# Kernel tuning notes

Measured on AMD Instinct MI355X. Metric: run time of the kernel, lower is better.

The kernel has to match this reference:

```python
import jax, jax.numpy as jnp
import numpy as np

B, T, D, H, L = 256, 512, 32, 128, 32


def gru_cell(x, h, Wih, Whh, bih, bhh):
    # PyTorch GRU cell: gates ordered (r, z, n)
    gi = x @ Wih.T + bih
    gh = h @ Whh.T + bhh
    ir, iz, inn = jnp.split(gi, 3, axis=-1)
    hr, hz, hn = jnp.split(gh, 3, axis=-1)
    r = jax.nn.sigmoid(ir + hr)
    z = jax.nn.sigmoid(iz + hz)
    n = jnp.tanh(inn + r * hn)
    return (1.0 - z) * n + z * h


def run_dir(x, lengths, Wih, Whh, bih, bhh):
    # Unidirectional GRU over padded batch; masked updates emulate packed sequences:
    # carry at the end equals the hidden state at each sequence's last valid step.
    Bb, Tt, _ = x.shape
    xT = jnp.swapaxes(x, 0, 1)                                   # [T,B,Din]
    mask = (jnp.arange(Tt)[:, None] < lengths[None, :])[:, :, None]  # [T,B,1]
    h0 = jnp.zeros((Bb, Whh.shape[1]), x.dtype)

    def step(h, inp):
        x_t, m = inp
        h_new = gru_cell(x_t, h, Wih, Whh, bih, bhh)
        h = jnp.where(m, h_new, h)
        return h, jnp.where(m, h_new, jnp.zeros_like(h_new))

    h_last, out = jax.lax.scan(step, h0, (xT, mask))
    return jnp.swapaxes(out, 0, 1), h_last


def reverse_seq(x, lengths):
    # Reverse each sequence within its own valid length (positions >= length are junk,
    # callers mask them out).
    Tt = x.shape[1]
    idx = jnp.clip(lengths[:, None] - 1 - jnp.arange(Tt)[None, :], 0)
    return jnp.take_along_axis(x, idx[:, :, None], axis=1)


def vrae_forward(x, eps, enc_Wih0, enc_Whh0, enc_bih0, enc_bhh0,
                 enc_Wih12, enc_Whh12, enc_bih12, enc_bhh12,
                 dec_Wih0, dec_Whh0, dec_bih0, dec_bhh0,
                 dec_Wih1, dec_Whh1, dec_bih1, dec_bhh1,
                 W_mean, b_mean, W_logvar, b_logvar,
                 W_z2h, b_z2h, W_out, b_out, lengths):
    Bb, Tt, _ = x.shape
    valid = (jnp.arange(Tt)[None, :] < lengths[:, None])[:, :, None].astype(x.dtype)

    # --- 3-layer bidirectional encoder (packed-sequence semantics) ---
    seq = x
    for l in range(3):
        if l == 0:
            pf = (enc_Wih0[0], enc_Whh0[0], enc_bih0[0], enc_bhh0[0])
            pb = (enc_Wih0[1], enc_Whh0[1], enc_bih0[1], enc_bhh0[1])
        else:
            pf = (enc_Wih12[l-1, 0], enc_Whh12[l-1, 0], enc_bih12[l-1, 0], enc_bhh12[l-1, 0])
            pb = (enc_Wih12[l-1, 1], enc_Whh12[l-1, 1], enc_bih12[l-1, 1], enc_bhh12[l-1, 1])
        out_f, h_f = run_dir(seq, lengths, *pf)
        out_b_rev, h_b = run_dir(reverse_seq(seq, lengths), lengths, *pb)
        out_b = reverse_seq(out_b_rev, lengths) * valid
        seq = jnp.concatenate([out_f, out_b], axis=-1)

    # hidden[-2] = last-layer forward final, hidden[-1] = last-layer backward final
    hcat = jnp.concatenate([h_f, h_b], axis=-1)                  # [B, 2H]
    mean = hcat @ W_mean.T + b_mean
    logvar = hcat @ W_logvar.T + b_logvar
    z = mean + jnp.exp(0.5 * logvar) * eps

    h_init = jnp.tanh(z @ W_z2h.T + b_z2h)                       # repeated over layers

    def dec_step(carry, _):
        d_in, h1, h2 = carry
        h1n = gru_cell(d_in, h1, dec_Wih0, dec_Whh0, dec_bih0, dec_bhh0)
        h2n = gru_cell(h1n, h2, dec_Wih1, dec_Whh1, dec_bih1, dec_bhh1)
        pred = h2n @ W_out.T + b_out
        return (pred, h1n, h2n), pred

    init = (jnp.zeros((Bb, x.shape[2]), x.dtype), h_init, h_init)
    _, preds = jax.lax.scan(dec_step, init, None, length=Tt)     # [T,B,D]
    reconstruction = jnp.swapaxes(preds, 0, 1)                   # [B,T,D]
    return reconstruction, mean, logvar


def setup_inputs() -> dict:
    key = jax.random.key(0)
    ks = jax.random.split(key, 32)
    s = 0.1
    inp = {}
    inp["x"] = jax.random.normal(ks[0], (B, T, D), jnp.float32)
    lengths = jnp.sort(jax.random.randint(ks[1], (B,), 1, T + 1))[::-1]
    inp["lengths"] = lengths.at[0].set(T).astype(jnp.int32)      # sorted desc, max == T
    inp["eps"] = jax.random.normal(ks[2], (B, L), jnp.float32)
    # encoder layer 0 (input D), stacked over directions [fwd, bwd]
    inp["enc_Wih0"] = jax.random.normal(ks[3], (2, 3 * H, D)) * s
    inp["enc_Whh0"] = jax.random.normal(ks[4], (2, 3 * H, H)) * s
    inp["enc_bih0"] = jax.random.normal(ks[5], (2, 3 * H)) * s
    inp["enc_bhh0"] = jax.random.normal(ks[6], (2, 3 * H)) * s
    # encoder layers 1..2 (input 2H), [layer, dir, ...]
    inp["enc_Wih12"] = jax.random.normal(ks[7], (2, 2, 3 * H, 2 * H)) * s
    inp["enc_Whh12"] = jax.random.normal(ks[8], (2, 2, 3 * H, H)) * s
    inp["enc_bih12"] = jax.random.normal(ks[9], (2, 2, 3 * H)) * s
    inp["enc_bhh12"] = jax.random.normal(ks[10], (2, 2, 3 * H)) * s
    # decoder layer 0 (input D) and layer 1 (input H)
    inp["dec_Wih0"] = jax.random.normal(ks[11], (3 * H, D)) * s
    inp["dec_Whh0"] = jax.random.normal(ks[12], (3 * H, H)) * s
    inp["dec_bih0"] = jax.random.normal(ks[13], (3 * H,)) * s
    inp["dec_bhh0"] = jax.random.normal(ks[14], (3 * H,)) * s
    inp["dec_Wih1"] = jax.random.normal(ks[15], (3 * H, H)) * s
    inp["dec_Whh1"] = jax.random.normal(ks[16], (3 * H, H)) * s
    inp["dec_bih1"] = jax.random.normal(ks[17], (3 * H,)) * s
    inp["dec_bhh1"] = jax.random.normal(ks[18], (3 * H,)) * s
    # linears
    inp["W_mean"] = jax.random.normal(ks[19], (L, 2 * H)) * s
    inp["b_mean"] = jax.random.normal(ks[20], (L,)) * s
    inp["W_logvar"] = jax.random.normal(ks[21], (L, 2 * H)) * s
    inp["b_logvar"] = jax.random.normal(ks[22], (L,)) * s
    inp["W_z2h"] = jax.random.normal(ks[23], (H, L)) * s
    inp["b_z2h"] = jax.random.normal(ks[24], (H,)) * s
    inp["W_out"] = jax.random.normal(ks[25], (D, H)) * s
    inp["b_out"] = jax.random.normal(ks[26], (D,)) * s
    return inp


def reference(x, lengths, eps, enc_Wih0, enc_Whh0, enc_bih0, enc_bhh0,
              enc_Wih12, enc_Whh12, enc_bih12, enc_bhh12,
              dec_Wih0, dec_Whh0, dec_bih0, dec_bhh0,
              dec_Wih1, dec_Whh1, dec_bih1, dec_bhh1,
              W_mean, b_mean, W_logvar, b_logvar,
              W_z2h, b_z2h, W_out, b_out):
    return vrae_forward(x, eps, enc_Wih0, enc_Whh0, enc_bih0, enc_bhh0,
                        enc_Wih12, enc_Whh12, enc_bih12, enc_bhh12,
                        dec_Wih0, dec_Whh0, dec_bih0, dec_bhh0,
                        dec_Wih1, dec_Whh1, dec_bih1, dec_bhh1,
                        W_mean, b_mean, W_logvar, b_logvar,
                        W_z2h, b_z2h, W_out, b_out, lengths)
```

## Files before the change

kernel.cpp:

```cpp
#include <hip/hip_runtime.h>
#include <hip/hip_bf16.h>


typedef __bf16 bf16;
typedef __bf16 bf16x8 __attribute__((ext_vector_type(8)));
typedef float f32x4 __attribute__((ext_vector_type(4)));

#define MFMA(a,b,c) __builtin_amdgcn_mfma_f32_16x16x32_bf16((a),(b),(c),0,0,0)
#define Z4 (f32x4){0.f,0.f,0.f,0.f}

__device__ __forceinline__ float sigm_(float x){ return 1.f/(1.f+__expf(-x)); }
__device__ __forceinline__ float tanh_(float x){
  x = fminf(15.f, fmaxf(-15.f, x));
  float e = __expf(2.f*x);
  return (e-1.f)/(e+1.f);
}
__device__ __forceinline__ float fin_(float v){ return (v - v == 0.0f) ? v : 0.0f; }
__device__ __forceinline__ void pina_(bf16x8 &v){ asm volatile("" : "+a"(v)); }

struct PrepJobs {
  const float* src[9];
  bf16* hi[9];
  bf16* lo[9];
  int n[9];
};

__global__ void prep_w(PrepJobs J){
  const int stride = gridDim.x*blockDim.x;
  const int t0 = blockIdx.x*blockDim.x + threadIdx.x;
  for (int j=0;j<9;++j){
    const float* __restrict__ s = J.src[j];
    bf16* __restrict__ h = J.hi[j];
    bf16* __restrict__ l = J.lo[j];
    const int n = J.n[j];
    for (int i=t0;i<n;i+=stride){
      float v = fin_(s[i]);
      bf16 hh = (bf16)v;
      h[i] = hh;
      l[i] = (bf16)(v - (float)hh);
    }
  }
}

template<int KIN, bool F32IN>
__global__ __launch_bounds__(512)
__attribute__((amdgpu_waves_per_eu(2, 2)))
void enc_rec(const void* __restrict__ seqIn_,
             bf16* __restrict__ seqOut,
             const bf16* __restrict__ WihHi_, const bf16* __restrict__ WihLo_,
             const bf16* __restrict__ WhhHi_, const bf16* __restrict__ WhhLo_,
             const float* __restrict__ bih_, const float* __restrict__ bhh_,
             const int* __restrict__ lengths,
             float* __restrict__ hFo, float* __restrict__ hBo)
{
  constexpr int NKS  = KIN/32;
  constexpr int XSTR = F32IN ? 40 : 264;
  constexpr int XPL  = 16*XSTR;
  constexpr int XSLOT= (F32IN?2:1)*XPL;
  const int tid = threadIdx.x;
  const int wave = tid>>6;
  const int lh   = tid&15;
  const int quad = (tid>>4)&3;
  const int dir  = blockIdx.x>>4;
  const int b0   = (blockIdx.x&15)*16;

  const bf16* __restrict__ WihHi = WihHi_ + (size_t)dir*384*KIN;
  const bf16* __restrict__ WihLo = WihLo_ + (size_t)dir*384*KIN;
  const bf16* __restrict__ WhhHi = WhhHi_ + (size_t)dir*384*128;
  const bf16* __restrict__ WhhLo = WhhLo_ + (size_t)dir*384*128;
  const float* __restrict__ bih = bih_ + dir*384;
  const float* __restrict__ bhh = bhh_ + dir*384;

  __shared__ bf16 hHi[16*136], hLo[16*136];
  __shared__ bf16 xb[4*XSLOT];

  const int jc = wave*16 + lh;
  const int cR = jc, cZ = 128+jc, cN = 256+jc;

  bf16x8 wRH[4],wRL[4],wZH[4],wZL[4],wNH[4],wNL[4];
#pragma unroll
  for (int ks=0;ks<4;++ks){
    const int o = ks*32 + quad*8;
    wRH[ks]=*(const bf16x8*)(WhhHi+(size_t)cR*128+o); wRL[ks]=*(const bf16x8*)(WhhLo+(size_t)cR*128+o);
    wZH[ks]=*(const bf16x8*)(WhhHi+(size_t)cZ*128+o); wZL[ks]=*(const bf16x8*)(WhhLo+(size_t)cZ*128+o);
    wNH[ks]=*(const bf16x8*)(WhhHi+(size_t)cN*128+o); wNL[ks]=*(const bf16x8*)(WhhLo+(size_t)cN*128+o);
    pina_(wRH[ks]); pina_(wRL[ks]); pina_(wZH[ks]); pina_(wZL[ks]); pina_(wNH[ks]); pina_(wNL[ks]);
  }
  const float bR  = bih[cR]+bhh[cR];
  const float bZc = bih[cZ]+bhh[cZ];
  const float bNi = bih[cN];
  const float bNh = bhh[cN];

  int lenRow[4];
#pragma unroll
  for (int r=0;r<4;++r) lenRow[r] = lengths[b0 + quad*4 + r];
  const int lenA = lengths[b0+lh];
  const int Tmax = lengths[b0];
  const int TT   = (Tmax+3)&~3;

  const int wrow = (tid>>4)&15;
  const int wcol = (tid&15)*8;
  const int lenW = lengths[b0 + wrow];
  const int srow = tid>>5;
  const int scol = tid&31;
  const int lenS = lengths[b0 + srow];

  for (int i=tid;i<16*136;i+=512){ hHi[i]=(bf16)0.f; hLo[i]=(bf16)0.f; }

  float hown[4] = {0.f,0.f,0.f,0.f};

  auto stage = [&](int slot, int sabs){
    int tb = dir ? (lenS-1-sabs) : sabs;
    tb = tb<0 ? 0 : (tb>511 ? 511 : tb);
    if constexpr (F32IN){
      float v = ((const float*)seqIn_)[((size_t)(b0+srow)*512+tb)*32 + scol];
      bf16 hh=(bf16)v;
      xb[slot*XSLOT + srow*XSTR + scol] = hh;
      xb[slot*XSLOT + XPL + srow*XSTR + scol] = (bf16)(v-(float)hh);
    } else {
      bf16x8 v = *(const bf16x8*)((const bf16*)seqIn_ + ((size_t)(b0+srow)*512+tb)*256 + scol*8);
      *(bf16x8*)&xb[slot*XSLOT + srow*XSTR + scol*8] = v;
    }
  };
#pragma unroll
  for (int s=0;s<4;++s) stage(s, 1+s);

  f32x4 accR[4], accZ[4], giN[4];
#pragma unroll
  for (int s=0;s<4;++s){ accR[s]=Z4; accZ[s]=Z4; giN[s]=Z4; }

  {
    int tb0 = dir ? (lenA-1) : 0; tb0 = tb0<0?0:tb0;
#pragma unroll
    for (int ks=0;ks<NKS;++ks){
      const int o = ks*32 + quad*8;
      bf16x8 axH, axL;
      if constexpr (F32IN){
        const float* ap = (const float*)seqIn_ + ((size_t)(b0+lh)*512+tb0)*KIN + o;
#pragma unroll
        for (int e=0;e<8;++e){ float v=ap[e]; bf16 hh=(bf16)v; axH[e]=hh; axL[e]=(bf16)(v-(float)hh); }
      } else {
        axH = *(const bf16x8*)((const bf16*)seqIn_ + ((size_t)(b0+lh)*512+tb0)*KIN + o);
      }
      bf16x8 bH, bL;
      bH=*(const bf16x8*)(WihHi+(size_t)cR*KIN+o); bL=*(const bf16x8*)(WihLo+(size_t)cR*KIN+o);
      accR[3]=MFMA(axH,bH,accR[3]); if constexpr(F32IN) accR[3]=MFMA(axL,bH,accR[3]); accR[3]=MFMA(axH,bL,accR[3]);
      bH=*(const bf16x8*)(WihHi+(size_t)cZ*KIN+o); bL=*(const bf16x8*)(WihLo+(size_t)cZ*KIN+o);
      accZ[3]=MFMA(axH,bH,accZ[3]); if constexpr(F32IN) accZ[3]=MFMA(axL,bH,accZ[3]); accZ[3]=MFMA(axH,bL,accZ[3]);
      bH=*(const bf16x8*)(WihHi+(size_t)cN*KIN+o); bL=*(const bf16x8*)(WihLo+(size_t)cN*KIN+o);
      giN[3]=MFMA(axH,bH,giN[3]);  if constexpr(F32IN) giN[3]=MFMA(axL,bH,giN[3]);  giN[3]=MFMA(axH,bL,giN[3]);
    }
  }
  __syncthreads();

  for (int t4=0; t4<TT; t4+=4){
#pragma unroll
    for (int p=0;p<4;++p){
      const int t = t4 + p;
      const int s = (p+3)&3;
      if (seqOut && tid<256 && t>0 && (t-1)<lenW){
        const int tp = t-1;
        const int tb = dir ? (lenW-1-tp) : tp;
        bf16x8 v = *(const bf16x8*)&hHi[wrow*136 + wcol];
        *(bf16x8*)(seqOut + ((size_t)(b0+wrow)*512 + tb)*256 + dir*128 + wcol) = v;
      }
      f32x4 gN = Z4;
#pragma unroll
      for (int ks=0;ks<4;++ks){
        bf16x8 aH = *(const bf16x8*)&hHi[lh*136 + ks*32 + quad*8];
        bf16x8 aL = *(const bf16x8*)&hLo[lh*136 + ks*32 + quad*8];
        accR[s]=MFMA(aH,wRH[ks],accR[s]); accR[s]=MFMA(aL,wRH[ks],accR[s]); accR[s]=MFMA(aH,wRL[ks],accR[s]);
        accZ[s]=MFMA(aH,wZH[ks],accZ[s]); accZ[s]=MFMA(aL,wZH[ks],accZ[s]); accZ[s]=MFMA(aH,wZL[ks],accZ[s]);
        gN     =MFMA(aH,wNH[ks],gN);      gN     =MFMA(aL,wNH[ks],gN);      gN     =MFMA(aH,wNL[ks],gN);
      }
      float hsel[4];
#pragma unroll
      for (int r=0;r<4;++r){
        float rr = sigm_(accR[s][r] + bR);
        float zz = sigm_(accZ[s][r] + bZc);
        float nn = tanh_(giN[s][r] + bNi + rr*(gN[r] + bNh));
        float hold = hown[r];
        float hnew = fin_((1.f-zz)*nn + zz*hold);
        hsel[r] = (t < lenRow[r]) ? hnew : hold;
        hown[r] = hsel[r];
      }
      if (p==0){
#pragma unroll
        for (int s2=0;s2<4;++s2){ accR[s2]=Z4; accZ[s2]=Z4; giN[s2]=Z4; }
#pragma unroll
        for (int ks=0;ks<NKS;++ks){
          const int o = ks*32 + quad*8;
          bf16x8 axH[4], axL[F32IN?4:1];
#pragma unroll
          for (int s2=0;s2<4;++s2){
            axH[s2] = *(const bf16x8*)&xb[s2*XSLOT + lh*XSTR + o];
            if constexpr (F32IN) axL[s2] = *(const bf16x8*)&xb[s2*XSLOT + XPL + lh*XSTR + o];
          }
          bf16x8 bH, bL;
          bH=*(const bf16x8*)(WihHi+(size_t)cR*KIN+o); bL=*(const bf16x8*)(WihLo+(size_t)cR*KIN+o);
#pragma unroll
          for (int s2=0;s2<4;++s2){
            accR[s2]=MFMA(axH[s2],bH,accR[s2]);
            if constexpr(F32IN) accR[s2]=MFMA(axL[s2],bH,accR[s2]);
            accR[s2]=MFMA(axH[s2],bL,accR[s2]);
          }
          bH=*(const bf16x8*)(WihHi+(size_t)cZ*KIN+o); bL=*(const bf16x8*)(WihLo+(size_t)cZ*KIN+o);
#pragma unroll
          for (int s2=0;s2<4;++s2){
            accZ[s2]=MFMA(axH[s2],bH,accZ[s2]);
            if constexpr(F32IN) accZ[s2]=MFMA(axL[s2],bH,accZ[s2]);
            accZ[s2]=MFMA(axH[s2],bL,accZ[s2]);
          }
          bH=*(const bf16x8*)(WihHi+(size_t)cN*KIN+o); bL=*(const bf16x8*)(WihLo+(size_t)cN*KIN+o);
#pragma unroll
          for (int s2=0;s2<4;++s2){
            giN[s2]=MFMA(axH[s2],bH,giN[s2]);
            if constexpr(F32IN) giN[s2]=MFMA(axL[s2],bH,giN[s2]);
            giN[s2]=MFMA(axH[s2],bL,giN[s2]);
          }
        }
      }
      __syncthreads();
#pragma unroll
      for (int r=0;r<4;++r){
        const int m = quad*4 + r;
        bf16 hi = (bf16)hsel[r];
        hHi[m*136+jc] = hi;
        hLo[m*136+jc] = (bf16)(hsel[r]-(float)hi);
      }
      if      (p==1){ stage(0, t4+5); stage(1, t4+6); }
      else if (p==2){ stage(2, t4+7); }
      else if (p==3){ stage(3, t4+8); }
      __syncthreads();
    }
  }
  if (seqOut && tid<256 && (TT-1)<lenW){
    const int tb = dir ? (lenW-1-(TT-1)) : (TT-1);
    bf16x8 v = *(const bf16x8*)&hHi[wrow*136 + wcol];
    *(bf16x8*)(seqOut + ((size_t)(b0+wrow)*512 + tb)*256 + dir*128 + wcol) = v;
  }
  float* hout = dir ? hBo : hFo;
  if (hout && tid<256){
#pragma unroll
    for (int e=0;e<8;++e){
      const int j = wcol+e;
      hout[(size_t)(b0+wrow)*128 + j] = fin_((float)hHi[wrow*136+j] + (float)hLo[wrow*136+j]);
    }
  }
}

__global__ void latent_k(const float* __restrict__ hF, const float* __restrict__ hB,
                         const float* __restrict__ eps,
                         const float* __restrict__ Wm, const float* __restrict__ bm,
                         const float* __restrict__ Wl, const float* __restrict__ bl,
                         const float* __restrict__ Wz, const float* __restrict__ bz,
                         float* __restrict__ out_mean, float* __restrict__ out_logvar,
                         float* __restrict__ hInit)
{
  const int b = blockIdx.x, tid = threadIdx.x;
  __shared__ float hc[256];
  __shared__ float mv[64];
  __shared__ float zz[32];
  for (int k=tid;k<256;k+=64) hc[k] = fin_((k<128)? hF[(size_t)b*128+k] : hB[(size_t)b*128+k-128]);
  __syncthreads();
  {
    const int i = tid & 31;
    const float* W = (tid<32)? Wm : Wl;
    float acc = (tid<32)? bm[i] : bl[i];
    for (int k=0;k<256;++k) acc += hc[k]*W[i*256+k];
    acc = fin_(acc);
    mv[tid] = acc;
    if (tid<32) out_mean[b*32+i] = acc;
    else        out_logvar[b*32+(tid-32)] = acc;
  }
  __syncthreads();
  if (tid<32) zz[tid] = fin_(mv[tid] + __expf(0.5f*mv[32+tid]) * eps[b*32+tid]);
  __syncthreads();
  for (int j=tid;j<128;j+=64){
    float a = bz[j];
    for (int k=0;k<32;++k) a += zz[k]*Wz[j*32+k];
    hInit[(size_t)b*128 + j] = tanh_(fin_(a));
  }
}

__global__ __launch_bounds__(512)
__attribute__((amdgpu_waves_per_eu(2, 2)))
void dec_rec(const float* __restrict__ hInit,
             const bf16* __restrict__ W0iH, const bf16* __restrict__ W0iL,
             const bf16* __restrict__ W0hH, const bf16* __restrict__ W0hL,
             const bf16* __restrict__ W1iH, const bf16* __restrict__ W1iL,
             const bf16* __restrict__ W1hH, const bf16* __restrict__ W1hL,
             const bf16* __restrict__ WoH,  const bf16* __restrict__ WoL,
             const float* __restrict__ bih0, const float* __restrict__ bhh0,
             const float* __restrict__ bih1, const float* __restrict__ bhh1,
             const float* __restrict__ bout,
             float* __restrict__ rec)
{
  const int tid = threadIdx.x;
  const int wave = tid>>6;
  const int lh   = tid&15;
  const int quad = (tid>>4)&3;
  const int b0 = blockIdx.x*16;
  const int jc = wave*16 + lh;
  const int cR = jc, cZ = 128+jc, cN = 256+jc;

  __shared__ bf16 h1H[16*136], h1L[16*136], h2H[16*136], h2L[16*136];
  __shared__ bf16 pH[16*40], pL[16*40];
  __shared__ bf16 w1iLds[384*128];
  __shared__ bf16 woHl[32*128], woLl[32*128];
  __shared__ bf16 w0iLds[384*32];

  const int sw1 = (jc&7)<<3;
  const int sw0 = (jc&3)<<3;
  const int swo = (lh&7)<<3;

  bf16x8 a0RH[4],a0RL[4],a0ZH[4],a0ZL[4],a0NH[4],a0NL[4];
  bf16x8 a1RH[4],a1RL[4],a1ZH[4],a1ZL[4],a1NH[4],a1NL[4];
#pragma unroll
  for (int ks=0;ks<4;++ks){
    const int o = ks*32 + quad*8;
    a0RH[ks]=*(const bf16x8*)(W0hH+(size_t)cR*128+o); a0RL[ks]=*(const bf16x8*)(W0hL+(size_t)cR*128+o);
    a0ZH[ks]=*(const bf16x8*)(W0hH+(size_t)cZ*128+o); a0ZL[ks]=*(const bf16x8*)(W0hL+(size_t)cZ*128+o);
    a0NH[ks]=*(const bf16x8*)(W0hH+(size_t)cN*128+o); a0NL[ks]=*(const bf16x8*)(W0hL+(size_t)cN*128+o);
    a1RH[ks]=*(const bf16x8*)(W1hH+(size_t)cR*128+o); a1RL[ks]=*(const bf16x8*)(W1hL+(size_t)cR*128+o);
    a1ZH[ks]=*(const bf16x8*)(W1hH+(size_t)cZ*128+o); a1ZL[ks]=*(const bf16x8*)(W1hL+(size_t)cZ*128+o);
    a1NH[ks]=*(const bf16x8*)(W1hH+(size_t)cN*128+o); a1NL[ks]=*(const bf16x8*)(W1hL+(size_t)cN*128+o);
    pina_(a0RH[ks]); pina_(a0RL[ks]); pina_(a0ZH[ks]); pina_(a0ZL[ks]); pina_(a0NH[ks]); pina_(a0NL[ks]);
    pina_(a1RH[ks]); pina_(a1RL[ks]); pina_(a1ZH[ks]); pina_(a1ZL[ks]); pina_(a1NH[ks]); pina_(a1NL[ks]);
  }
  const float b1R = bih0[cR]+bhh0[cR], b1Z = bih0[cZ]+bhh0[cZ], b1Ni = bih0[cN], b1Nh = bhh0[cN];
  const float b2R = bih1[cR]+bhh1[cR], b2Z = bih1[cZ]+bhh1[cZ], b2Ni = bih1[cN], b2Nh = bhh1[cN];
  const float bo = (wave<2) ? bout[wave*16+lh] : 0.f;

  for (int i=tid; i<384*16; i+=512){
    const int rr = i>>4, k8 = (i&15)*8;
    *(bf16x8*)&w1iLds[rr*128 + (k8 ^ ((rr&7)<<3))] = *(const bf16x8*)(W1iH + (size_t)rr*128 + k8);
  }
  for (int i=tid; i<32*16; i+=512){
    const int rr = i>>4, k8 = (i&15)*8;
    const int c = rr*128 + (k8 ^ ((rr&7)<<3));
    *(bf16x8*)&woHl[c] = *(const bf16x8*)(WoH + (size_t)rr*128 + k8);
    *(bf16x8*)&woLl[c] = *(const bf16x8*)(WoL + (size_t)rr*128 + k8);
  }
  for (int i=tid; i<384*4; i+=512){
    const int rr = i>>2, k8 = (i&3)*8;
    *(bf16x8*)&w0iLds[rr*32 + (k8 ^ ((rr&3)<<3))] = *(const bf16x8*)(W0iH + (size_t)rr*32 + k8);
  }
  float h1own[4], h2own[4];
#pragma unroll
  for (int r=0;r<4;++r){
    float v = fin_(hInit[(size_t)(b0+quad*4+r)*128 + jc]);
    h1own[r]=v; h2own[r]=v;
  }
  if (tid < 256){
    const int row = (tid>>4)&15;
    const int c0  = (tid&15)*8;
#pragma unroll
    for (int e=0;e<8;++e){
      const int j = c0+e;
      float v = fin_(hInit[(size_t)(b0+row)*128 + j]);
      bf16 hi=(bf16)v, lo=(bf16)(v-(float)hi);
      h1H[row*136+j]=hi; h1L[row*136+j]=lo;
      h2H[row*136+j]=hi; h2L[row*136+j]=lo;
    }
  }
  for (int i=tid;i<16*40;i+=512){ pH[i]=(bf16)0.f; pL[i]=(bf16)0.f; }
  __syncthreads();

  f32x4 c1R, c1Z, c1Nh, c2R, c2Z, c2Nh;

  auto ghpre = [&](){
    c1R=Z4; c1Z=Z4; c1Nh=Z4; c2R=Z4; c2Z=Z4; c2Nh=Z4;
#pragma unroll
    for (int ks=0;ks<4;++ks){
      const int o = ks*32 + quad*8;
      bf16x8 aH = *(const bf16x8*)&h1H[lh*136 + o];
      bf16x8 aL = *(const bf16x8*)&h1L[lh*136 + o];
      c1R =MFMA(aH,a0RH[ks],c1R);  c1R =MFMA(aL,a0RH[ks],c1R);  c1R =MFMA(aH,a0RL[ks],c1R);
      c1Z =MFMA(aH,a0ZH[ks],c1Z);  c1Z =MFMA(aL,a0ZH[ks],c1Z);  c1Z =MFMA(aH,a0ZL[ks],c1Z);
      c1Nh=MFMA(aH,a0NH[ks],c1Nh); c1Nh=MFMA(aL,a0NH[ks],c1Nh); c1Nh=MFMA(aH,a0NL[ks],c1Nh);
    }
#pragma unroll
    for (int ks=0;ks<4;++ks){
      const int o = ks*32 + quad*8;
      bf16x8 aH = *(const bf16x8*)&h2H[lh*136 + o];
      bf16x8 aL = *(const bf16x8*)&h2L[lh*136 + o];
      c2R =MFMA(aH,a1RH[ks],c2R);  c2R =MFMA(aL,a1RH[ks],c2R);  c2R =MFMA(aH,a1RL[ks],c2R);
      c2Z =MFMA(aH,a1ZH[ks],c2Z);  c2Z =MFMA(aL,a1ZH[ks],c2Z);  c2Z =MFMA(aH,a1ZL[ks],c2Z);
      c2Nh=MFMA(aH,a1NH[ks],c2Nh); c2Nh=MFMA(aL,a1NH[ks],c2Nh); c2Nh=MFMA(aH,a1NL[ks],c2Nh);
    }
  };
  ghpre();

  for (int t=0;t<512;++t){
    {
      f32x4 c1Ni = Z4;
      bf16x8 aP0 = *(const bf16x8*)&pH[lh*40 + quad*8];
      bf16x8 aP1 = *(const bf16x8*)&pL[lh*40 + quad*8];
      const int o = quad*8;
      bf16x8 bH,bL;
      bH=*(const bf16x8*)&w0iLds[cR*32 + (o^sw0)]; bL=*(const bf16x8*)(W0iL+(size_t)cR*32+o);
      c1R=MFMA(aP0,bH,c1R); c1R=MFMA(aP1,bH,c1R); c1R=MFMA(aP0,bL,c1R);
      bH=*(const bf16x8*)&w0iLds[cZ*32 + (o^sw0)]; bL=*(const bf16x8*)(W0iL+(size_t)cZ*32+o);
      c1Z=MFMA(aP0,bH,c1Z); c1Z=MFMA(aP1,bH,c1Z); c1Z=MFMA(aP0,bL,c1Z);
      bH=*(const bf16x8*)&w0iLds[cN*32 + (o^sw0)]; bL=*(const bf16x8*)(W0iL+(size_t)cN*32+o);
      c1Ni=MFMA(aP0,bH,c1Ni); c1Ni=MFMA(aP1,bH,c1Ni); c1Ni=MFMA(aP0,bL,c1Ni);
#pragma unroll
      for (int r=0;r<4;++r){
        const int m = quad*4+r;
        float rr = sigm_(c1R[r] + b1R);
        float z  = sigm_(c1Z[r] + b1Z);
        float nn = tanh_(c1Ni[r] + b1Ni + rr*(c1Nh[r] + b1Nh));
        float hnew = fin_((1.f-z)*nn + z*h1own[r]);
        h1own[r] = hnew;
        bf16 hi=(bf16)hnew;
        h1H[m*136+jc]=hi; h1L[m*136+jc]=(bf16)(hnew-(float)hi);
      }
    }
    __syncthreads();
    {
      f32x4 c2Ni = Z4;
#pragma unroll
      for (int ks=0;ks<4;++ks){
        const int o = ks*32 + quad*8;
        bf16x8 aH = *(const bf16x8*)&h1H[lh*136 + o];
        bf16x8 aL = *(const bf16x8*)&h1L[lh*136 + o];
        bf16x8 bH,bL;
        bH=*(const bf16x8*)&w1iLds[cR*128+(o^sw1)]; bL=*(const bf16x8*)(W1iL+(size_t)cR*128+o);
        c2R=MFMA(aH,bH,c2R); c2R=MFMA(aL,bH,c2R); c2R=MFMA(aH,bL,c2R);
        bH=*(const bf16x8*)&w1iLds[cZ*128+(o^sw1)]; bL=*(const bf16x8*)(W1iL+(size_t)cZ*128+o);
        c2Z=MFMA(aH,bH,c2Z); c2Z=MFMA(aL,bH,c2Z); c2Z=MFMA(aH,bL,c2Z);
        bH=*(const bf16x8*)&w1iLds[cN*128+(o^sw1)]; bL=*(const bf16x8*)(W1iL+(size_t)cN*128+o);
        c2Ni=MFMA(aH,bH,c2Ni); c2Ni=MFMA(aL,bH,c2Ni); c2Ni=MFMA(aH,bL,c2Ni);
      }
#pragma unroll
      for (int r=0;r<4;++r){
        const int m = quad*4+r;
        float rr = sigm_(c2R[r] + b2R);
        float z  = sigm_(c2Z[r] + b2Z);
        float nn = tanh_(c2Ni[r] + b2Ni + rr*(c2Nh[r] + b2Nh));
        float hnew = fin_((1.f-z)*nn + z*h2own[r]);
        h2own[r] = hnew;
        bf16 hi=(bf16)hnew;
        h2H[m*136+jc]=hi; h2L[m*136+jc]=(bf16)(hnew-(float)hi);
      }
    }
    __syncthreads();
    if (wave<2){
      f32x4 po=Z4;
#pragma unroll
      for (int ks=0;ks<4;++ks){
        const int o = ks*32 + quad*8;
        bf16x8 oH = *(const bf16x8*)&h2H[lh*136 + o];
        bf16x8 oL = *(const bf16x8*)&h2L[lh*136 + o];
        const int wc = (wave*16+lh)*128 + (o^swo);
        bf16x8 bH = *(const bf16x8*)&woHl[wc];
        bf16x8 bL = *(const bf16x8*)&woLl[wc];
        po=MFMA(oH,bH,po); po=MFMA(oL,bH,po); po=MFMA(oH,bL,po);
      }
#pragma unroll
      for (int r=0;r<4;++r){
        const int m = quad*4+r;
        float pv = fin_(po[r]+bo);
        rec[((size_t)(b0+m)*512 + t)*32 + wave*16+lh] = pv;
        bf16 hi=(bf16)pv;
        pH[m*40 + wave*16+lh]=hi; pL[m*40 + wave*16+lh]=(bf16)(pv-(float)hi);
      }
    }
    if (t+1 < 512) ghpre();
    __syncthreads();
  }
}

extern "C" void kernel_launch(void* const* d_in, const int* in_sizes, int n_in,
                              void* d_out, int out_size, void* d_ws, size_t ws_size,
                              hipStream_t stream)
{
  const float* x       = (const float*)d_in[0];
  const int*   lengths = (const int*)d_in[1];
  const float* eps     = (const float*)d_in[2];
  const float* eWih0   = (const float*)d_in[3];
  const float* eWhh0   = (const float*)d_in[4];
  const float* ebih0   = (const float*)d_in[5];
  const float* ebhh0   = (const float*)d_in[6];
  const float* eWih12  = (const float*)d_in[7];
  const float* eWhh12  = (const float*)d_in[8];
  const float* ebih12  = (const float*)d_in[9];
  const float* ebhh12  = (const float*)d_in[10];
  const float* dWih0   = (const float*)d_in[11];
  const float* dWhh0   = (const float*)d_in[12];
  const float* dbih0   = (const float*)d_in[13];
  const float* dbhh0   = (const float*)d_in[14];
  const float* dWih1   = (const float*)d_in[15];
  const float* dWhh1   = (const float*)d_in[16];
  const float* dbih1   = (const float*)d_in[17];
  const float* dbhh1   = (const float*)d_in[18];
  const float* Wm      = (const float*)d_in[19];
  const float* bm      = (const float*)d_in[20];
  const float* Wl      = (const float*)d_in[21];
  const float* bl      = (const float*)d_in[22];
  const float* Wz      = (const float*)d_in[23];
  const float* bz      = (const float*)d_in[24];
  const float* Wo      = (const float*)d_in[25];
  const float* bo      = (const float*)d_in[26];

  char* ws = (char*)d_ws;
  bf16* P     = (bf16*)ws;
  bf16* seqA  = (bf16*)(ws + (size_t)(4<<20));
  bf16* seqB  = (bf16*)(ws + (size_t)(68<<20));
  float* hF    = (float*)seqA;
  float* hB    = hF + 256*128;
  float* hInit = hB + 256*128;

  const size_t O_eWih0  = 0;
  const size_t O_eWhh0  = 49152;
  const size_t O_eWih12 = 245760;
  const size_t O_eWhh12 = 1032192;
  const size_t O_dWih0  = 1425408;
  const size_t O_dWhh0  = 1449984;
  const size_t O_dWih1  = 1548288;
  const size_t O_dWhh1  = 1646592;
  const size_t O_Wout   = 1744896;

  float* out   = (float*)d_out;
  float* rec   = out;
  float* omean = out + (size_t)4194304;
  float* ologv = omean + 8192;

  size_t zoff = (size_t)(4<<20);
  size_t zbytes = (size_t)(128<<20);
  if (zoff + zbytes > ws_size) zbytes = (ws_size > zoff)? ws_size - zoff : 0;
  hipMemsetAsync(ws + zoff, 0, zbytes, stream);

  PrepJobs J;
  const float* srcs[9] = {eWih0, eWhh0, eWih12, eWhh12, dWih0, dWhh0, dWih1, dWhh1, Wo};
  const size_t offs[9] = {O_eWih0,O_eWhh0,O_eWih12,O_eWhh12,O_dWih0,O_dWhh0,O_dWih1,O_dWhh1,O_Wout};
  const int    ns[9]   = {24576, 98304, 393216, 196608, 12288, 49152, 49152, 49152, 4096};
  for (int j=0;j<9;++j){ J.src[j]=srcs[j]; J.hi[j]=P+offs[j]; J.lo[j]=P+offs[j]+ns[j]; J.n[j]=ns[j]; }
  prep_w<<<256, 256, 0, stream>>>(J);

  dim3 blk(512);

  enc_rec<32,true><<<32, blk, 0, stream>>>(x, seqA,
      P+O_eWih0, P+O_eWih0+24576, P+O_eWhh0, P+O_eWhh0+98304,
      ebih0, ebhh0, lengths, nullptr, nullptr);
  enc_rec<256,false><<<32, blk, 0, stream>>>(seqA, seqB,
      P+O_eWih12, P+O_eWih12+393216, P+O_eWhh12, P+O_eWhh12+196608,
      ebih12, ebhh12, lengths, nullptr, nullptr);
  enc_rec<256,false><<<32, blk, 0, stream>>>(seqB, nullptr,
      P+O_eWih12+196608, P+O_eWih12+393216+196608,
      P+O_eWhh12+98304,  P+O_eWhh12+196608+98304,
      ebih12+768, ebhh12+768, lengths, hF, hB);
  latent_k<<<256, 64, 0, stream>>>(hF, hB, eps, Wm, bm, Wl, bl, Wz, bz,
                                   omean, ologv, hInit);
  dec_rec<<<16, blk, 0, stream>>>(hInit,
      P+O_dWih0, P+O_dWih0+12288, P+O_dWhh0, P+O_dWhh0+49152,
      P+O_dWih1, P+O_dWih1+49152, P+O_dWhh1, P+O_dWhh1+49152,
      P+O_Wout,  P+O_Wout+4096,
      dbih0, dbhh0, dbih1, dbhh1, bo, rec);
}
```

Baseline: 9.967 ms.

## Double-buffer encoder hidden state in LDS and rebalance decoder weight registers

The encoder's shared hidden-state buffers become ping-pong double buffers. Each step reads one copy and writes the other, which removes one of the two block-wide barriers per timestep. In the decoder, some layer-0 recurrent weight fragments are pinned to VGPRs instead of AGPRs, and the N-gate low fragment is reloaded from global memory inside ghpre. This is meant to relieve register pressure, at the cost of an extra global load per k-step.

```diff
diff --git a/kernel.cpp b/kernel.cpp
--- a/kernel.cpp
+++ b/kernel.cpp
@@ -16,6 +16,7 @@
   return (e-1.f)/(e+1.f);
 }
 __device__ __forceinline__ float fin_(float v){ return (v - v == 0.0f) ? v : 0.0f; }
+__device__ __forceinline__ void pinv_(bf16x8 &v){ asm volatile("" : "+v"(v)); }
 __device__ __forceinline__ void pina_(bf16x8 &v){ asm volatile("" : "+a"(v)); }
 
 struct PrepJobs {
@@ -71,7 +72,7 @@
   const float* __restrict__ bih = bih_ + dir*384;
   const float* __restrict__ bhh = bhh_ + dir*384;
 
-  __shared__ bf16 hHi[16*136], hLo[16*136];
+  __shared__ bf16 hHi[2][16*136], hLo[2][16*136];
   __shared__ bf16 xb[4*XSLOT];
 
   const int jc = wave*16 + lh;
@@ -105,7 +106,7 @@
   const int scol = tid&31;
   const int lenS = lengths[b0 + srow];
 
-  for (int i=tid;i<16*136;i+=512){ hHi[i]=(bf16)0.f; hLo[i]=(bf16)0.f; }
+  for (int i=tid;i<2*16*136;i+=512){ hHi[0][i]=(bf16)0.f; hLo[0][i]=(bf16)0.f; }
 
   float hown[4] = {0.f,0.f,0.f,0.f};
 
@@ -158,17 +159,19 @@
     for (int p=0;p<4;++p){
       const int t = t4 + p;
       const int s = (p+3)&3;
+      const int rp = (p+1)&1;
+      const int wp = p&1;
       if (seqOut && tid<256 && t>0 && (t-1)<lenW){
         const int tp = t-1;
         const int tb = dir ? (lenW-1-tp) : tp;
-        bf16x8 v = *(const bf16x8*)&hHi[wrow*136 + wcol];
+        bf16x8 v = *(const bf16x8*)&hHi[rp][wrow*136 + wcol];
         *(bf16x8*)(seqOut + ((size_t)(b0+wrow)*512 + tb)*256 + dir*128 + wcol) = v;
       }
       f32x4 gN = Z4;
 #pragma unroll
       for (int ks=0;ks<4;++ks){
-        bf16x8 aH = *(const bf16x8*)&hHi[lh*136 + ks*32 + quad*8];
-        bf16x8 aL = *(const bf16x8*)&hLo[lh*136 + ks*32 + quad*8];
+        bf16x8 aH = *(const bf16x8*)&hHi[rp][lh*136 + ks*32 + quad*8];
+        bf16x8 aL = *(const bf16x8*)&hLo[rp][lh*136 + ks*32 + quad*8];
         accR[s]=MFMA(aH,wRH[ks],accR[s]); accR[s]=MFMA(aL,wRH[ks],accR[s]); accR[s]=MFMA(aH,wRL[ks],accR[s]);
         accZ[s]=MFMA(aH,wZH[ks],accZ[s]); accZ[s]=MFMA(aL,wZH[ks],accZ[s]); accZ[s]=MFMA(aH,wZL[ks],accZ[s]);
         gN     =MFMA(aH,wNH[ks],gN);      gN     =MFMA(aL,wNH[ks],gN);      gN     =MFMA(aH,wNL[ks],gN);
@@ -220,13 +223,12 @@
           }
         }
       }
-      __syncthreads();
 #pragma unroll
       for (int r=0;r<4;++r){
         const int m = quad*4 + r;
         bf16 hi = (bf16)hsel[r];
-        hHi[m*136+jc] = hi;
-        hLo[m*136+jc] = (bf16)(hsel[r]-(float)hi);
+        hHi[wp][m*136+jc] = hi;
+        hLo[wp][m*136+jc] = (bf16)(hsel[r]-(float)hi);
       }
       if      (p==1){ stage(0, t4+5); stage(1, t4+6); }
       else if (p==2){ stage(2, t4+7); }
@@ -236,7 +238,7 @@
   }
   if (seqOut && tid<256 && (TT-1)<lenW){
     const int tb = dir ? (lenW-1-(TT-1)) : (TT-1);
-    bf16x8 v = *(const bf16x8*)&hHi[wrow*136 + wcol];
+    bf16x8 v = *(const bf16x8*)&hHi[1][wrow*136 + wcol];
     *(bf16x8*)(seqOut + ((size_t)(b0+wrow)*512 + tb)*256 + dir*128 + wcol) = v;
   }
   float* hout = dir ? hBo : hFo;
@@ -244,7 +246,7 @@
 #pragma unroll
     for (int e=0;e<8;++e){
       const int j = wcol+e;
-      hout[(size_t)(b0+wrow)*128 + j] = fin_((float)hHi[wrow*136+j] + (float)hLo[wrow*136+j]);
+      hout[(size_t)(b0+wrow)*128 + j] = fin_((float)hHi[1][wrow*136+j] + (float)hLo[1][wrow*136+j]);
     }
   }
 }
@@ -314,19 +316,21 @@
   const int sw0 = (jc&3)<<3;
   const int swo = (lh&7)<<3;
 
-  bf16x8 a0RH[4],a0RL[4],a0ZH[4],a0ZL[4],a0NH[4],a0NL[4];
   bf16x8 a1RH[4],a1RL[4],a1ZH[4],a1ZL[4],a1NH[4],a1NL[4];
+  bf16x8 a0RH[4],a0RL[4];
+  bf16x8 a0ZH[4],a0ZL[4],a0NH[4];
 #pragma unroll
   for (int ks=0;ks<4;++ks){
     const int o = ks*32 + quad*8;
     a0RH[ks]=*(const bf16x8*)(W0hH+(size_t)cR*128+o); a0RL[ks]=*(const bf16x8*)(W0hL+(size_t)cR*128+o);
     a0ZH[ks]=*(const bf16x8*)(W0hH+(size_t)cZ*128+o); a0ZL[ks]=*(const bf16x8*)(W0hL+(size_t)cZ*128+o);
-    a0NH[ks]=*(const bf16x8*)(W0hH+(size_t)cN*128+o); a0NL[ks]=*(const bf16x8*)(W0hL+(size_t)cN*128+o);
+    a0NH[ks]=*(const bf16x8*)(W0hH+(size_t)cN*128+o);
     a1RH[ks]=*(const bf16x8*)(W1hH+(size_t)cR*128+o); a1RL[ks]=*(const bf16x8*)(W1hL+(size_t)cR*128+o);
     a1ZH[ks]=*(const bf16x8*)(W1hH+(size_t)cZ*128+o); a1ZL[ks]=*(const bf16x8*)(W1hL+(size_t)cZ*128+o);
     a1NH[ks]=*(const bf16x8*)(W1hH+(size_t)cN*128+o); a1NL[ks]=*(const bf16x8*)(W1hL+(size_t)cN*128+o);
-    pina_(a0RH[ks]); pina_(a0RL[ks]); pina_(a0ZH[ks]); pina_(a0ZL[ks]); pina_(a0NH[ks]); pina_(a0NL[ks]);
     pina_(a1RH[ks]); pina_(a1RL[ks]); pina_(a1ZH[ks]); pina_(a1ZL[ks]); pina_(a1NH[ks]); pina_(a1NL[ks]);
+    pina_(a0RH[ks]); pina_(a0RL[ks]);
+    pinv_(a0ZH[ks]); pinv_(a0ZL[ks]); pinv_(a0NH[ks]);
   }
   const float b1R = bih0[cR]+bhh0[cR], b1Z = bih0[cZ]+bhh0[cZ], b1Ni = bih0[cN], b1Nh = bhh0[cN];
   const float b2R = bih1[cR]+bhh1[cR], b2Z = bih1[cZ]+bhh1[cZ], b2Ni = bih1[cN], b2Nh = bhh1[cN];
@@ -376,9 +380,10 @@
       const int o = ks*32 + quad*8;
       bf16x8 aH = *(const bf16x8*)&h1H[lh*136 + o];
       bf16x8 aL = *(const bf16x8*)&h1L[lh*136 + o];
+      bf16x8 nl = *(const bf16x8*)(W0hL+(size_t)cN*128+o);
       c1R =MFMA(aH,a0RH[ks],c1R);  c1R =MFMA(aL,a0RH[ks],c1R);  c1R =MFMA(aH,a0RL[ks],c1R);
       c1Z =MFMA(aH,a0ZH[ks],c1Z);  c1Z =MFMA(aL,a0ZH[ks],c1Z);  c1Z =MFMA(aH,a0ZL[ks],c1Z);
-      c1Nh=MFMA(aH,a0NH[ks],c1Nh); c1Nh=MFMA(aL,a0NH[ks],c1Nh); c1Nh=MFMA(aH,a0NL[ks],c1Nh);
+      c1Nh=MFMA(aH,a0NH[ks],c1Nh); c1Nh=MFMA(aL,a0NH[ks],c1Nh); c1Nh=MFMA(aH,nl,c1Nh);
     }
 #pragma unroll
     for (int ks=0;ks<4;++ks){
```

Result: no change. 9.988 ms (+0.2%).
